# Kernel tuning notes

Measured on AMD Instinct MI355X. Metric: run time of the kernel, lower is better.

Reference implementation:

```python
import jax, jax.numpy as jnp
import numpy as np

LEAK = 0.95          # leak_rate
SPECTRAL_RADIUS = 1.2
SPARSITY = 0.1
EPS_LN = 1e-5


def _ln(x, g, b):
    m = jnp.mean(x, axis=-1, keepdims=True)
    v = jnp.var(x, axis=-1, keepdims=True)
    return (x - m) / jnp.sqrt(v + EPS_LN) * g + b


def setup_inputs() -> dict:
    key = jax.random.key(0)
    ks = jax.random.split(key, 12)
    Bsz, S, D, H = 8, 2048, 512, 1024
    x = jax.random.normal(ks[0], (Bsz, S, D), jnp.float32)
    # frozen reservoir weights
    W_in = jax.random.uniform(ks[1], (H, D), jnp.float32, -1.0, 1.0) / jnp.sqrt(D)
    W_res = jax.random.normal(ks[2], (H, H), jnp.float32)
    mask = (jax.random.uniform(ks[3], (H, H)) > SPARSITY).astype(jnp.float32)
    W_res = W_res * mask
    # circular-law estimate of spectral radius for sparse gaussian matrix
    est_radius = jnp.sqrt(H * (1.0 - SPARSITY))
    W_res = W_res * (SPECTRAL_RADIUS / est_radius)
    # SSM branch params
    A = -jnp.ones((H,), jnp.float32) * 10.0
    W_B = jax.random.normal(ks[4], (H, D), jnp.float32) / jnp.sqrt(D)
    w_delta = jax.random.normal(ks[5], (D,), jnp.float32) / jnp.sqrt(D)
    b_delta = jnp.zeros((), jnp.float32)
    # readout (shared by both branches)
    ro_g = jnp.ones((H,), jnp.float32)
    ro_b = jnp.zeros((H,), jnp.float32)
    W_ro = jax.random.normal(ks[6], (D, H), jnp.float32) / jnp.sqrt(H)
    b_ro = jnp.zeros((D,), jnp.float32)
    # gate + input norm
    W_gate = jax.random.normal(ks[7], (D, D), jnp.float32) / jnp.sqrt(D)
    b_gate = jnp.zeros((D,), jnp.float32)
    norm_g = jnp.ones((D,), jnp.float32)
    norm_b = jnp.zeros((D,), jnp.float32)
    return {"x": x, "norm_g": norm_g, "norm_b": norm_b, "W_in": W_in,
            "W_res": W_res, "A": A, "W_B": W_B, "w_delta": w_delta,
            "b_delta": b_delta, "ro_g": ro_g, "ro_b": ro_b, "W_ro": W_ro,
            "b_ro": b_ro, "W_gate": W_gate, "b_gate": b_gate}


def reference(x, norm_g, norm_b, W_in, W_res, A, W_B, w_delta, b_delta,
              ro_g, ro_b, W_ro, b_ro, W_gate, b_gate):
    Bsz, S, D = x.shape
    H = W_in.shape[0]
    x_norm = _ln(x, norm_g, norm_b)

    # ---- TrueReservoir: precompute input projection, scan the recurrence ----
    xin = jnp.einsum('bsd,hd->sbh', x_norm, W_in)  # (S, B, H)
    h0 = jnp.zeros((Bsz, H), x.dtype)

    def res_step(prev, xt):
        new = jnp.tanh(xt + prev @ W_res.T)
        new = LEAK * new + (1.0 - LEAK) * prev
        return new, new

    _, res_states = jax.lax.scan(res_step, h0, xin)        # (S, B, H)
    res_states = jnp.swapaxes(res_states, 0, 1)            # (B, S, H)

    def readout(s):
        return jax.nn.gelu(_ln(s, ro_g, ro_b) @ W_ro.T + b_ro, approximate=False)

    reservoir_out = readout(res_states)                    # (B, S, D)

    # ---- diagonal SSM branch ----
    Bm = jnp.einsum('bsd,hd->bsh', x_norm, W_B)            # (B, S, H)
    delta = jax.nn.softplus(jnp.einsum('bsd,d->bs', x_norm, w_delta) + b_delta)
    A_bar = jnp.exp(A * delta[..., None])                  # (B, S, H)
    B_bar = Bm * (1.0 - A_bar) / (A + 1e-8)

    def ssm_step(prev, ab_bb):
        ab, bb = ab_bb
        h = ab * prev + bb
        return h, h

    _, ssm_states = jax.lax.scan(
        ssm_step, h0,
        (jnp.swapaxes(A_bar, 0, 1), jnp.swapaxes(B_bar, 0, 1)))
    ssm_states = jnp.swapaxes(ssm_states, 0, 1)            # (B, S, H)
    ssm_out = readout(ssm_states)                          # (B, S, D)

    # ---- gated fusion ----
    gate = jax.nn.sigmoid(x @ W_gate.T + b_gate)           # (B, S, D)
    return reservoir_out * gate + ssm_out * (1.0 - gate)
```

## Files before the change

kernel.cpp:

```cpp
#include <hip/hip_runtime.h>
#include <math.h>

#define S_LEN 2048
#define BATCH 8
#define DIM   512
#define HID   1024

static const size_t OFF_XIN   = 0;
static const size_t OFF_BM    = 16777216;
static const size_t OFF_RES   = 33554432;
static const size_t OFF_MEAN  = 50331648;
static const size_t OFF_RSTD  = 50348032;
static const size_t OFF_DELTA = 50364416;
static const size_t OFF_AC    = 50380800;
static const size_t OFF_BC    = 50642944;
static const size_t OFF_HST   = 50905088;
static const size_t OFF_HBUF  = 51167232;
static const size_t OFF_BAR   = 51183616;

__global__ __launch_bounds__(128) void ln_stats_kernel(
    const float* __restrict__ x, const float* __restrict__ g, const float* __restrict__ b,
    const float* __restrict__ wd, const float* __restrict__ bd,
    float* __restrict__ meanO, float* __restrict__ rstdO, float* __restrict__ deltaO)
{
    const int m = blockIdx.x;
    const int tid = threadIdx.x;
    float4 v = ((const float4*)(x + (size_t)m * DIM))[tid];
    float s1 = v.x + v.y + v.z + v.w;
    float s2 = v.x*v.x + v.y*v.y + v.z*v.z + v.w*v.w;
    #pragma unroll
    for (int o = 1; o < 64; o <<= 1) { s1 += __shfl_xor(s1, o); s2 += __shfl_xor(s2, o); }
    __shared__ float sA[4];
    if ((tid & 63) == 0) { sA[tid >> 6] = s1; sA[2 + (tid >> 6)] = s2; }
    __syncthreads();
    s1 = sA[0] + sA[1]; s2 = sA[2] + sA[3];
    const float mean = s1 * (1.0f / DIM);
    const float var  = s2 * (1.0f / DIM) - mean * mean;
    const float rstd = 1.0f / sqrtf(var + 1e-5f);
    float4 gv = ((const float4*)g)[tid];
    float4 bv = ((const float4*)b)[tid];
    float4 wv = ((const float4*)wd)[tid];
    float y0 = (v.x - mean) * rstd * gv.x + bv.x;
    float y1 = (v.y - mean) * rstd * gv.y + bv.y;
    float y2 = (v.z - mean) * rstd * gv.z + bv.z;
    float y3 = (v.w - mean) * rstd * gv.w + bv.w;
    float dd = y0*wv.x + y1*wv.y + y2*wv.z + y3*wv.w;
    #pragma unroll
    for (int o = 1; o < 64; o <<= 1) dd += __shfl_xor(dd, o);
    __shared__ float sB[2];
    if ((tid & 63) == 0) sB[tid >> 6] = dd;
    __syncthreads();
    if (tid == 0) {
        meanO[m] = mean;
        rstdO[m] = rstd;
        float t = sB[0] + sB[1] + bd[0];
        deltaO[m] = fmaxf(t, 0.0f) + log1pf(expf(-fabsf(t)));
    }
}

template<int EPI, bool LNA>
__global__ __launch_bounds__(256) void sgemm_bt(
    const float* __restrict__ A, const float* __restrict__ Bw,
    float* __restrict__ C, const float* __restrict__ bias,
    const float* __restrict__ lnMean, const float* __restrict__ lnRstd,
    const float* __restrict__ lnG, const float* __restrict__ lnB,
    int M, int N, int K)
{
    __shared__ __align__(16) float As[16][128];
    __shared__ __align__(16) float Bs[16][128];
    const int tid = threadIdx.x;
    const int tx = tid & 15, ty = tid >> 4;
    const size_t bm = blockIdx.x, bn = blockIdx.y;
    const float* Ab = A  + bm * 128 * (size_t)K;
    const float* Bb = Bw + bn * 128 * (size_t)K;
    const int lr = tid >> 1;
    const int lk = (tid & 1) * 8;
    float mu = 0.0f, rs = 0.0f;
    if (LNA) { mu = lnMean[bm * 128 + lr]; rs = lnRstd[bm * 128 + lr]; }
    float acc[8][8] = {};
    for (int kt = 0; kt < K; kt += 16) {
        float4 a0 = *(const float4*)(Ab + (size_t)lr * K + kt + lk);
        float4 a1 = *(const float4*)(Ab + (size_t)lr * K + kt + lk + 4);
        float4 b0 = *(const float4*)(Bb + (size_t)lr * K + kt + lk);
        float4 b1 = *(const float4*)(Bb + (size_t)lr * K + kt + lk + 4);
        if (LNA) {
            float4 g0 = *(const float4*)(lnG + kt + lk);
            float4 g1 = *(const float4*)(lnG + kt + lk + 4);
            float4 h0 = *(const float4*)(lnB + kt + lk);
            float4 h1 = *(const float4*)(lnB + kt + lk + 4);
            a0.x = (a0.x - mu) * rs * g0.x + h0.x;  a0.y = (a0.y - mu) * rs * g0.y + h0.y;
            a0.z = (a0.z - mu) * rs * g0.z + h0.z;  a0.w = (a0.w - mu) * rs * g0.w + h0.w;
            a1.x = (a1.x - mu) * rs * g1.x + h1.x;  a1.y = (a1.y - mu) * rs * g1.y + h1.y;
            a1.z = (a1.z - mu) * rs * g1.z + h1.z;  a1.w = (a1.w - mu) * rs * g1.w + h1.w;
        }
        __syncthreads();
        As[lk+0][lr]=a0.x; As[lk+1][lr]=a0.y; As[lk+2][lr]=a0.z; As[lk+3][lr]=a0.w;
        As[lk+4][lr]=a1.x; As[lk+5][lr]=a1.y; As[lk+6][lr]=a1.z; As[lk+7][lr]=a1.w;
        Bs[lk+0][lr]=b0.x; Bs[lk+1][lr]=b0.y; Bs[lk+2][lr]=b0.z; Bs[lk+3][lr]=b0.w;
        Bs[lk+4][lr]=b1.x; Bs[lk+5][lr]=b1.y; Bs[lk+6][lr]=b1.z; Bs[lk+7][lr]=b1.w;
        __syncthreads();
        #pragma unroll
        for (int kk = 0; kk < 16; ++kk) {
            float av[8], bv[8];
            *(float4*)&av[0] = *(const float4*)&As[kk][ty*8];
            *(float4*)&av[4] = *(const float4*)&As[kk][ty*8+4];
            *(float4*)&bv[0] = *(const float4*)&Bs[kk][tx*8];
            *(float4*)&bv[4] = *(const float4*)&Bs[kk][tx*8+4];
            #pragma unroll
            for (int i = 0; i < 8; ++i)
                #pragma unroll
                for (int j = 0; j < 8; ++j)
                    acc[i][j] = fmaf(av[i], bv[j], acc[i][j]);
        }
    }
    const size_t crow = bm * 128 + ty * 8;
    const size_t ccol = bn * 128 + tx * 8;
    float bs8[8];
    if (EPI == 2 || EPI == 3) {
        #pragma unroll
        for (int j = 0; j < 8; ++j) bs8[j] = bias[ccol + j];
    }
    #pragma unroll
    for (int i = 0; i < 8; ++i) {
        #pragma unroll
        for (int j = 0; j < 8; ++j) {
            const size_t idx = (crow + i) * (size_t)N + ccol + j;
            float v = acc[i][j];
            if (EPI == 0) {
                C[idx] = v;
            } else if (EPI == 2) {
                float z = v + bs8[j];
                C[idx] = 1.0f / (1.0f + expf(-z));
            } else {
                float z = v + bs8[j];
                C[idx] = 0.5f * z * (1.0f + erff(z * 0.70710678118654752f));
            }
        }
    }
}

__global__ __launch_bounds__(512) void reservoir_scan(
    const float* __restrict__ xin, const float* __restrict__ Wres,
    float* __restrict__ res, float* __restrict__ hbuf, unsigned int* __restrict__ bar)
{
    __shared__ __align__(16) float hl[HID];
    const int b   = blockIdx.x & 7;
    const int w   = blockIdx.x >> 3;
    const int tid = threadIdx.x;
    const int r   = tid >> 4;
    const int l   = tid & 15;
    const int row = w * 32 + r;

    float4 wreg[16];
    {
        const float* Wr = Wres + (size_t)row * HID;
        #pragma unroll
        for (int i = 0; i < 16; ++i)
            wreg[i] = *(const float4*)(Wr + i * 64 + l * 4);
    }
    if (tid < 256) ((float4*)hl)[tid] = float4{0.f, 0.f, 0.f, 0.f};
    __syncthreads();

    const float* xb = xin + (size_t)b * S_LEN * HID;
    float*       rb = res + (size_t)b * S_LEN * HID;
    unsigned int* gflags = bar + (size_t)b * 1024;
    unsigned int* myflag = gflags + (size_t)w * 32;
    unsigned long long* hb64 = (unsigned long long*)hbuf;

    float xv = (l == 0) ? xb[row] : 0.0f;

    for (int t = 0; t < S_LEN; ++t) {
        float xnext = (l == 0 && t + 1 < S_LEN) ? xb[(size_t)(t + 1) * HID + row] : 0.0f;

        float acc = 0.0f;
        #pragma unroll
        for (int i = 0; i < 16; ++i) {
            float4 hv = *(const float4*)(hl + i * 64 + l * 4);
            acc = fmaf(wreg[i].x, hv.x, acc);
            acc = fmaf(wreg[i].y, hv.y, acc);
            acc = fmaf(wreg[i].z, hv.z, acc);
            acc = fmaf(wreg[i].w, hv.w, acc);
        }
        #pragma unroll
        for (int o = 1; o < 16; o <<= 1) acc += __shfl_xor(acc, o);

        if (l == 0) {
            float nh = 0.95f * tanhf(xv + acc) + 0.05f * hl[row];
            rb[(size_t)t * HID + row] = nh;
            __hip_atomic_store(
                hbuf + ((t + 1) & 1) * (BATCH * HID) + b * HID + row, nh,
                __ATOMIC_RELAXED, __HIP_MEMORY_SCOPE_AGENT);
        }
        xv = xnext;

        __syncthreads();
        if (tid == 0)
            __hip_atomic_store(myflag, (unsigned int)(t + 1),
                               __ATOMIC_RELAXED, __HIP_MEMORY_SCOPE_AGENT);
        if (tid < 64) {
            const unsigned int target = (unsigned int)(t + 1);
            bool done = (tid >= 32);
            while (true) {
                if (!done)
                    done = __hip_atomic_load(gflags + (size_t)tid * 32,
                                             __ATOMIC_RELAXED, __HIP_MEMORY_SCOPE_AGENT) >= target;
                if (__all(done)) break;
                __builtin_amdgcn_s_sleep(1);
            }
        }
        __syncthreads();

        if (t + 1 < S_LEN) {
            unsigned long long v = __hip_atomic_load(
                hb64 + ((size_t)((t + 1) & 1)) * (BATCH * HID / 2) + (size_t)b * (HID / 2) + tid,
                __ATOMIC_RELAXED, __HIP_MEMORY_SCOPE_AGENT);
            ((unsigned long long*)hl)[tid] = v;
            __syncthreads();
        }
    }
}

__global__ __launch_bounds__(1024) void ssm_chunk(
    const float* __restrict__ Bm, const float* __restrict__ delta,
    const float* __restrict__ Avec, float* __restrict__ Ac, float* __restrict__ Bc)
{
    const int blk = blockIdx.x;
    const int b = blk >> 5, c = blk & 31, h = threadIdx.x;
    const float A = Avec[h];
    const float invA = 1.0f / (A + 1e-8f);
    const int m0 = b * S_LEN + c * 64;
    const size_t base = (size_t)m0 * HID + h;
    float ap = 1.0f, acc = 0.0f;
    for (int s = 0; s < 64; ++s) {
        float a  = expf(A * delta[m0 + s]);
        float bb = Bm[base + (size_t)s * HID] * (1.0f - a) * invA;
        acc = a * acc + bb;
        ap *= a;
    }
    Ac[(size_t)blk * HID + h] = ap;
    Bc[(size_t)blk * HID + h] = acc;
}

__global__ __launch_bounds__(1024) void ssm_chain(
    const float* __restrict__ Ac, const float* __restrict__ Bc, float* __restrict__ hst)
{
    const int b = blockIdx.x, h = threadIdx.x;
    float hs = 0.0f;
    for (int c = 0; c < 32; ++c) {
        size_t idx = ((size_t)b * 32 + c) * HID + h;
        hst[idx] = hs;
        hs = Ac[idx] * hs + Bc[idx];
    }
}

__global__ __launch_bounds__(1024) void ssm_expand(
    float* __restrict__ Bm, const float* __restrict__ delta,
    const float* __restrict__ Avec, const float* __restrict__ hst)
{
    const int blk = blockIdx.x;
    const int b = blk >> 5, c = blk & 31, h = threadIdx.x;
    const float A = Avec[h];
    const float invA = 1.0f / (A + 1e-8f);
    const int m0 = b * S_LEN + c * 64;
    const size_t base = (size_t)m0 * HID + h;
    float hv = hst[(size_t)blk * HID + h];
    for (int s = 0; s < 64; ++s) {
        float a  = expf(A * delta[m0 + s]);
        float bb = Bm[base + (size_t)s * HID] * (1.0f - a) * invA;
        hv = a * hv + bb;
        Bm[base + (size_t)s * HID] = hv;
    }
}

__global__ __launch_bounds__(256) void ln_h_kernel(
    float* __restrict__ st, const float* __restrict__ g, const float* __restrict__ bb)
{
    const int m = blockIdx.x, tid = threadIdx.x;
    float* rowp = st + (size_t)m * HID;
    float4 v = ((const float4*)rowp)[tid];
    float s1 = v.x + v.y + v.z + v.w;
    float s2 = v.x*v.x + v.y*v.y + v.z*v.z + v.w*v.w;
    #pragma unroll
    for (int o = 1; o < 64; o <<= 1) { s1 += __shfl_xor(s1, o); s2 += __shfl_xor(s2, o); }
    __shared__ float sh[8];
    if ((tid & 63) == 0) { sh[tid >> 6] = s1; sh[4 + (tid >> 6)] = s2; }
    __syncthreads();
    s1 = sh[0] + sh[1] + sh[2] + sh[3];
    s2 = sh[4] + sh[5] + sh[6] + sh[7];
    const float mean = s1 * (1.0f / HID);
    const float var  = s2 * (1.0f / HID) - mean * mean;
    const float rstd = 1.0f / sqrtf(var + 1e-5f);
    float4 gv = ((const float4*)g)[tid];
    float4 bv = ((const float4*)bb)[tid];
    float4 y;
    y.x = (v.x - mean) * rstd * gv.x + bv.x;
    y.y = (v.y - mean) * rstd * gv.y + bv.y;
    y.z = (v.z - mean) * rstd * gv.z + bv.z;
    y.w = (v.w - mean) * rstd * gv.w + bv.w;
    ((float4*)rowp)[tid] = y;
}

__global__ __launch_bounds__(256) void fuse_kernel(
    const float* __restrict__ y, const float* __restrict__ gate, float* __restrict__ out)
{
    const int i = blockIdx.x * 256 + threadIdx.x;
    float4 ys = ((const float4*)y)[i];
    float4 yr = ((const float4*)y)[i + 2097152];
    float4 g  = ((const float4*)gate)[i];
    float4 o;
    o.x = yr.x * g.x + ys.x * (1.0f - g.x);
    o.y = yr.y * g.y + ys.y * (1.0f - g.y);
    o.z = yr.z * g.z + ys.z * (1.0f - g.z);
    o.w = yr.w * g.w + ys.w * (1.0f - g.w);
    ((float4*)out)[i] = o;
}

extern "C" void kernel_launch(void* const* d_in, const int* in_sizes, int n_in,
                              void* d_out, int out_size, void* d_ws, size_t ws_size,
                              hipStream_t stream)
{
    const float* x       = (const float*)d_in[0];
    const float* norm_g  = (const float*)d_in[1];
    const float* norm_b  = (const float*)d_in[2];
    const float* W_in    = (const float*)d_in[3];
    const float* W_res   = (const float*)d_in[4];
    const float* Avec    = (const float*)d_in[5];
    const float* W_B     = (const float*)d_in[6];
    const float* w_delta = (const float*)d_in[7];
    const float* b_delta = (const float*)d_in[8];
    const float* ro_g    = (const float*)d_in[9];
    const float* ro_b    = (const float*)d_in[10];
    const float* W_ro    = (const float*)d_in[11];
    const float* b_ro    = (const float*)d_in[12];
    const float* W_gate  = (const float*)d_in[13];
    const float* b_gate  = (const float*)d_in[14];
    float* out = (float*)d_out;

    float* W = (float*)d_ws;
    float* xin   = W + OFF_XIN;
    float* Bm    = W + OFF_BM;
    float* resS  = W + OFF_RES;
    float* meanB = W + OFF_MEAN;
    float* rstdB = W + OFF_RSTD;
    float* delta = W + OFF_DELTA;
    float* Ac    = W + OFF_AC;
    float* Bc    = W + OFF_BC;
    float* hst   = W + OFF_HST;
    float* hbuf  = W + OFF_HBUF;
    unsigned int* bar = (unsigned int*)(W + OFF_BAR);
    float* stacked = Bm;
    float* ybuf    = W + OFF_XIN;
    float* gbuf    = W + OFF_RES;

    ln_stats_kernel<<<16384, 128, 0, stream>>>(x, norm_g, norm_b, w_delta, b_delta,
                                               meanB, rstdB, delta);
    sgemm_bt<0, true><<<dim3(128, 8), 256, 0, stream>>>(
        x, W_in, xin, nullptr, meanB, rstdB, norm_g, norm_b, 16384, 1024, 512);
    sgemm_bt<0, true><<<dim3(128, 8), 256, 0, stream>>>(
        x, W_B, Bm, nullptr, meanB, rstdB, norm_g, norm_b, 16384, 1024, 512);
    (void)hipMemsetAsync(bar, 0, 8192 * sizeof(unsigned int), stream);
    reservoir_scan<<<256, 512, 0, stream>>>(xin, W_res, resS, hbuf, bar);
    ssm_chunk<<<256, 1024, 0, stream>>>(Bm, delta, Avec, Ac, Bc);
    ssm_chain<<<8, 1024, 0, stream>>>(Ac, Bc, hst);
    ssm_expand<<<256, 1024, 0, stream>>>(Bm, delta, Avec, hst);
    ln_h_kernel<<<32768, 256, 0, stream>>>(stacked, ro_g, ro_b);
    sgemm_bt<3, false><<<dim3(256, 4), 256, 0, stream>>>(
        stacked, W_ro, ybuf, b_ro, nullptr, nullptr, nullptr, nullptr, 32768, 512, 1024);
    sgemm_bt<2, false><<<dim3(128, 4), 256, 0, stream>>>(
        x, W_gate, gbuf, b_gate, nullptr, nullptr, nullptr, nullptr, 16384, 512, 512);
    fuse_kernel<<<8192, 256, 0, stream>>>(ybuf, gbuf, out);
}
```

Measured before the change: 5.211 ms.

## Replace flag barrier with timestep-tagged state packets in reservoir scan

Drops the per-step global flag barrier between workgroups in the reservoir recurrence. Each hidden value is now published as a 64-bit packet that carries the timestep alongside the float, and consumers spin directly on the packets they need. This removes a separate flag write, a polling loop and one block-wide barrier from every step of the serial critical path. In exchange every thread polls two global words and the hidden-state buffer doubles in size. The weight registers are also unrolled into named variables, which should not change the generated code.

```diff
diff --git a/kernel.cpp b/kernel.cpp
--- a/kernel.cpp
+++ b/kernel.cpp
@@ -16,7 +16,6 @@
 static const size_t OFF_BC    = 50642944;
 static const size_t OFF_HST   = 50905088;
 static const size_t OFF_HBUF  = 51167232;
-static const size_t OFF_BAR   = 51183616;
 
 __global__ __launch_bounds__(128) void ln_stats_kernel(
     const float* __restrict__ x, const float* __restrict__ g, const float* __restrict__ b,
@@ -141,7 +140,7 @@
 
 __global__ __launch_bounds__(512) void reservoir_scan(
     const float* __restrict__ xin, const float* __restrict__ Wres,
-    float* __restrict__ res, float* __restrict__ hbuf, unsigned int* __restrict__ bar)
+    float* __restrict__ res, unsigned long long* __restrict__ hb)
 {
     __shared__ __align__(16) float hl[HID];
     const int b   = blockIdx.x & 7;
@@ -151,21 +150,21 @@
     const int l   = tid & 15;
     const int row = w * 32 + r;
 
-    float4 wreg[16];
-    {
-        const float* Wr = Wres + (size_t)row * HID;
-        #pragma unroll
-        for (int i = 0; i < 16; ++i)
-            wreg[i] = *(const float4*)(Wr + i * 64 + l * 4);
-    }
+    const float* Wr = Wres + (size_t)row * HID + l * 4;
+    float4 w0  = *(const float4*)(Wr + 0*64),  w1  = *(const float4*)(Wr + 1*64);
+    float4 w2  = *(const float4*)(Wr + 2*64),  w3  = *(const float4*)(Wr + 3*64);
+    float4 w4  = *(const float4*)(Wr + 4*64),  w5  = *(const float4*)(Wr + 5*64);
+    float4 w6  = *(const float4*)(Wr + 6*64),  w7  = *(const float4*)(Wr + 7*64);
+    float4 w8  = *(const float4*)(Wr + 8*64),  w9  = *(const float4*)(Wr + 9*64);
+    float4 w10 = *(const float4*)(Wr + 10*64), w11 = *(const float4*)(Wr + 11*64);
+    float4 w12 = *(const float4*)(Wr + 12*64), w13 = *(const float4*)(Wr + 13*64);
+    float4 w14 = *(const float4*)(Wr + 14*64), w15 = *(const float4*)(Wr + 15*64);
+
     if (tid < 256) ((float4*)hl)[tid] = float4{0.f, 0.f, 0.f, 0.f};
     __syncthreads();
 
     const float* xb = xin + (size_t)b * S_LEN * HID;
     float*       rb = res + (size_t)b * S_LEN * HID;
-    unsigned int* gflags = bar + (size_t)b * 1024;
-    unsigned int* myflag = gflags + (size_t)w * 32;
-    unsigned long long* hb64 = (unsigned long long*)hbuf;
 
     float xv = (l == 0) ? xb[row] : 0.0f;
 
@@ -173,48 +172,49 @@
         float xnext = (l == 0 && t + 1 < S_LEN) ? xb[(size_t)(t + 1) * HID + row] : 0.0f;
 
         float acc = 0.0f;
-        #pragma unroll
-        for (int i = 0; i < 16; ++i) {
-            float4 hv = *(const float4*)(hl + i * 64 + l * 4);
-            acc = fmaf(wreg[i].x, hv.x, acc);
-            acc = fmaf(wreg[i].y, hv.y, acc);
-            acc = fmaf(wreg[i].z, hv.z, acc);
-            acc = fmaf(wreg[i].w, hv.w, acc);
-        }
+        const float* hp = hl + l * 4;
+        #define DOT(i, W) { float4 hv = *(const float4*)(hp + i*64); \
+            acc = fmaf(W.x, hv.x, acc); acc = fmaf(W.y, hv.y, acc);  \
+            acc = fmaf(W.z, hv.z, acc); acc = fmaf(W.w, hv.w, acc); }
+        DOT(0,w0) DOT(1,w1) DOT(2,w2) DOT(3,w3) DOT(4,w4) DOT(5,w5) DOT(6,w6) DOT(7,w7)
+        DOT(8,w8) DOT(9,w9) DOT(10,w10) DOT(11,w11) DOT(12,w12) DOT(13,w13) DOT(14,w14) DOT(15,w15)
+        #undef DOT
         #pragma unroll
         for (int o = 1; o < 16; o <<= 1) acc += __shfl_xor(acc, o);
 
         if (l == 0) {
             float nh = 0.95f * tanhf(xv + acc) + 0.05f * hl[row];
             rb[(size_t)t * HID + row] = nh;
-            __hip_atomic_store(
-                hbuf + ((t + 1) & 1) * (BATCH * HID) + b * HID + row, nh,
-                __ATOMIC_RELAXED, __HIP_MEMORY_SCOPE_AGENT);
+            if (t + 1 < S_LEN) {
+                unsigned long long pkt =
+                    (unsigned long long)__float_as_uint(nh) |
+                    ((unsigned long long)(unsigned)(t + 1) << 32);
+                __hip_atomic_store(
+                    hb + (size_t)((t + 1) & 1) * (BATCH * HID) + (size_t)b * HID + row,
+                    pkt, __ATOMIC_RELAXED, __HIP_MEMORY_SCOPE_AGENT);
+            }
         }
         xv = xnext;
+        asm volatile("" ::: "memory");
 
         __syncthreads();
-        if (tid == 0)
-            __hip_atomic_store(myflag, (unsigned int)(t + 1),
-                               __ATOMIC_RELAXED, __HIP_MEMORY_SCOPE_AGENT);
-        if (tid < 64) {
-            const unsigned int target = (unsigned int)(t + 1);
-            bool done = (tid >= 32);
-            while (true) {
-                if (!done)
-                    done = __hip_atomic_load(gflags + (size_t)tid * 32,
-                                             __ATOMIC_RELAXED, __HIP_MEMORY_SCOPE_AGENT) >= target;
-                if (__all(done)) break;
-                __builtin_amdgcn_s_sleep(1);
-            }
-        }
-        __syncthreads();
 
         if (t + 1 < S_LEN) {
-            unsigned long long v = __hip_atomic_load(
-                hb64 + ((size_t)((t + 1) & 1)) * (BATCH * HID / 2) + (size_t)b * (HID / 2) + tid,
-                __ATOMIC_RELAXED, __HIP_MEMORY_SCOPE_AGENT);
-            ((unsigned long long*)hl)[tid] = v;
+            const unsigned tgt = (unsigned)(t + 1);
+            unsigned long long* src =
+                hb + (size_t)((t + 1) & 1) * (BATCH * HID) + (size_t)b * HID;
+            unsigned long long v0 = 0, v1 = 0;
+            bool d0 = false, d1 = false;
+            do {
+                if (!d0) v0 = __hip_atomic_load(src + tid,
+                                __ATOMIC_RELAXED, __HIP_MEMORY_SCOPE_AGENT);
+                if (!d1) v1 = __hip_atomic_load(src + tid + 512,
+                                __ATOMIC_RELAXED, __HIP_MEMORY_SCOPE_AGENT);
+                d0 = d0 || (unsigned)(v0 >> 32) >= tgt;
+                d1 = d1 || (unsigned)(v1 >> 32) >= tgt;
+            } while (!(d0 && d1));
+            hl[tid]       = __uint_as_float((unsigned)v0);
+            hl[tid + 512] = __uint_as_float((unsigned)v1);
             __syncthreads();
         }
     }
@@ -346,8 +346,7 @@
     float* Ac    = W + OFF_AC;
     float* Bc    = W + OFF_BC;
     float* hst   = W + OFF_HST;
-    float* hbuf  = W + OFF_HBUF;
-    unsigned int* bar = (unsigned int*)(W + OFF_BAR);
+    unsigned long long* hb = (unsigned long long*)(W + OFF_HBUF);
     float* stacked = Bm;
     float* ybuf    = W + OFF_XIN;
     float* gbuf    = W + OFF_RES;
@@ -358,8 +357,8 @@
         x, W_in, xin, nullptr, meanB, rstdB, norm_g, norm_b, 16384, 1024, 512);
     sgemm_bt<0, true><<<dim3(128, 8), 256, 0, stream>>>(
         x, W_B, Bm, nullptr, meanB, rstdB, norm_g, norm_b, 16384, 1024, 512);
-    (void)hipMemsetAsync(bar, 0, 8192 * sizeof(unsigned int), stream);
-    reservoir_scan<<<256, 512, 0, stream>>>(xin, W_res, resS, hbuf, bar);
+    (void)hipMemsetAsync(hb, 0, 2 * BATCH * HID * sizeof(unsigned long long), stream);
+    reservoir_scan<<<256, 512, 0, stream>>>(xin, W_res, resS, hb);
     ssm_chunk<<<256, 1024, 0, stream>>>(Bm, delta, Avec, Ac, Bc);
     ssm_chain<<<8, 1024, 0, stream>>>(Ac, Bc, hst);
     ssm_expand<<<256, 1024, 0, stream>>>(Bm, delta, Avec, hst);
```

Measured after the change: 6.924 ms. 32.9% more time.
